# Kernel optimization log

Hardware: AMD Instinct MI355X
Metric: run time of the kernel (lower is better)

Reference implementation:

```python
import jax, jax.numpy as jnp
import numpy as np

B, T, D, F_FF, E, TOP_K = 8, 2048, 1024, 4096, 8, 2
CAP_FACTOR = 1.25


def setup_inputs() -> dict:
    key = jax.random.key(0)
    ks = jax.random.split(key, 7)
    s = 0.02
    return {
        "x": jax.random.normal(ks[0], (B, T, D), dtype=jnp.float32),
        "w_router": jax.random.normal(ks[1], (D, E), dtype=jnp.float32) * s,
        "b_router": jnp.zeros((E,), dtype=jnp.float32),
        "w1": jax.random.normal(ks[2], (E, D, F_FF), dtype=jnp.float32) * s,
        "b1": jnp.zeros((E, F_FF), dtype=jnp.float32),
        "w2": jax.random.normal(ks[3], (E, F_FF, D), dtype=jnp.float32) * s,
        "b2": jnp.zeros((E, D), dtype=jnp.float32),
    }


def reference(x, w_router, b_router, w1, b1, w2, b2):
    b, t, d = x.shape
    n = b * t
    e = w_router.shape[1]
    xf = x.reshape(n, d)

    # router in float32 (as original: .float())
    logits = xf.astype(jnp.float32) @ w_router + b_router
    gates = jax.nn.softmax(logits, axis=-1)              # [N, E]
    topv, topi = jax.lax.top_k(gates, TOP_K)             # [N, K]

    cap = max(1, int(CAP_FACTOR * n / e))

    # flatten assignments in (token, slot) order -> matches python loop order
    e_flat = topi.reshape(-1)                            # [N*K] expert id
    g_flat = topv.reshape(-1)                            # [N*K] gate value
    tok = jnp.repeat(jnp.arange(n), TOP_K)               # [N*K] token id

    # position of each assignment inside its expert (arrival order)
    onehot = jax.nn.one_hot(e_flat, e, dtype=jnp.int32)  # [N*K, E]
    pos = jnp.cumsum(onehot, axis=0)[jnp.arange(n * TOP_K), e_flat] - 1
    keep = pos < cap                                     # capacity dropping
    posc = jnp.minimum(pos, cap - 1)

    # dispatch: [E, cap, D] buffers (unique kept slots -> scatter-add safe)
    buf = jnp.zeros((e, cap, d), x.dtype).at[e_flat, posc].add(
        jnp.where(keep[:, None], xf[tok], 0.0))

    # per-expert FFN as grouped GEMM (exact GELU, as torch nn.GELU default)
    h = jax.nn.gelu(jnp.einsum('ecd,edf->ecf', buf, w1) + b1[:, None, :],
                    approximate=False)
    out = jnp.einsum('ecf,efd->ecd', h, w2) + b2[:, None, :]

    # combine: weighted scatter-add back to tokens
    og = out[e_flat, posc]                               # [N*K, D]
    w = jnp.where(keep, g_flat, 0.0).astype(x.dtype)
    y = jnp.zeros((n, d), x.dtype).at[tok].add(w[:, None] * og)
    ws = jnp.zeros((n,), x.dtype).at[tok].add(w)
    y = jnp.where((ws > 0.0)[:, None], y / jnp.maximum(ws, 1e-6)[:, None], y)
    return y.reshape(b, t, d)
```

## Files before the change

### kernel.cpp

```cpp
#include <hip/hip_runtime.h>

#define NTOK   16384
#define DMODEL 1024
#define FFF    4096
#define NEXP   8
#define CAP    2560
#define NASSIGN (NTOK*2)

typedef __bf16 bf16x8 __attribute__((ext_vector_type(8)));
typedef float  f32x4  __attribute__((ext_vector_type(4)));

__device__ __forceinline__ unsigned short f2bf(float f) {
    unsigned int u = __float_as_uint(f);
    u = u + 0x7FFFu + ((u >> 16) & 1u);
    return (unsigned short)(u >> 16);
}
__device__ __forceinline__ float bf2f(unsigned short s) {
    return __uint_as_float(((unsigned int)s) << 16);
}

__global__ void router_kernel(const float* __restrict__ x,
                              const float* __restrict__ wr,
                              const float* __restrict__ br,
                              int* __restrict__ topi,
                              float* __restrict__ topv) {
    int t    = blockIdx.x * 4 + (threadIdx.x >> 6);
    int lane = threadIdx.x & 63;
    const float* xr = x + (size_t)t * DMODEL;
    float a[8] = {0.f,0.f,0.f,0.f,0.f,0.f,0.f,0.f};
    for (int d = lane; d < DMODEL; d += 64) {
        float xv = xr[d];
        const float* w = wr + d * 8;
        #pragma unroll
        for (int e = 0; e < 8; e++) a[e] = fmaf(xv, w[e], a[e]);
    }
    #pragma unroll
    for (int off = 32; off > 0; off >>= 1) {
        #pragma unroll
        for (int e = 0; e < 8; e++) a[e] += __shfl_xor(a[e], off, 64);
    }
    if (lane == 0) {
        float l[8], g[8];
        float mx = -1e30f;
        #pragma unroll
        for (int e = 0; e < 8; e++) { l[e] = a[e] + br[e]; mx = fmaxf(mx, l[e]); }
        float s = 0.f;
        #pragma unroll
        for (int e = 0; e < 8; e++) { g[e] = expf(l[e] - mx); s += g[e]; }
        float inv = 1.f / s;
        #pragma unroll
        for (int e = 0; e < 8; e++) g[e] *= inv;
        float v1 = -1.f, v2 = -1.f; int i1 = 0, i2 = 0;
        #pragma unroll
        for (int e = 0; e < 8; e++) {
            float v = g[e];
            if (v > v1)      { v2 = v1; i2 = i1; v1 = v; i1 = e; }
            else if (v > v2) { v2 = v; i2 = e; }
        }
        topi[t*2]   = i1; topi[t*2+1] = i2;
        topv[t*2]   = v1; topv[t*2+1] = v2;
    }
}

__global__ void scan_kernel(const int* __restrict__ topi,
                            int* __restrict__ pos,
                            int* __restrict__ slot_tok,
                            int* __restrict__ kept) {
    const int APT = NASSIGN / 256;
    int tid = threadIdx.x, lane = tid & 63, w = tid >> 6;
    int base = tid * APT;
    int c[8] = {0,0,0,0,0,0,0,0};
    for (int i = 0; i < APT; i++) {
        int e = topi[base + i];
        #pragma unroll
        for (int q = 0; q < 8; q++) c[q] += (e == q);
    }
    int excl[8], wtot[8];
    #pragma unroll
    for (int e = 0; e < 8; e++) {
        int s = c[e];
        for (int off = 1; off < 64; off <<= 1) {
            int n = __shfl_up(s, off, 64);
            if (lane >= off) s += n;
        }
        excl[e] = s - c[e];
        wtot[e] = __shfl(s, 63, 64);
    }
    __shared__ int woff[4][8];
    if (lane == 0) {
        #pragma unroll
        for (int e = 0; e < 8; e++) woff[w][e] = wtot[e];
    }
    __syncthreads();
    if (tid == 0) {
        for (int e = 0; e < 8; e++) {
            int run = 0;
            for (int ww = 0; ww < 4; ww++) { int t0 = woff[ww][e]; woff[ww][e] = run; run += t0; }
            kept[e] = run < CAP ? run : CAP;
        }
    }
    __syncthreads();
    int run[8];
    #pragma unroll
    for (int e = 0; e < 8; e++) run[e] = woff[w][e] + excl[e];
    for (int i = 0; i < APT; i++) {
        int a = base + i;
        int e = topi[a];
        int p = 0;
        #pragma unroll
        for (int q = 0; q < 8; q++) if (e == q) { p = run[q]; run[q] = p + 1; }
        pos[a] = p;
        if (p < CAP) slot_tok[(size_t)e * CAP + p] = a >> 1;
    }
}

__global__ void dispatch_kernel(const float* __restrict__ x,
                                const int* __restrict__ slot_tok,
                                const int* __restrict__ kept,
                                unsigned short* __restrict__ xb) {
    int row  = blockIdx.x * 4 + (threadIdx.x >> 6);
    int lane = threadIdx.x & 63;
    int e = row / CAP;
    int p = row - e * CAP;
    if (p >= kept[e]) return;
    int t = slot_tok[row];
    const float4* src = reinterpret_cast<const float4*>(x + (size_t)t * DMODEL);
    ushort4* dst = reinterpret_cast<ushort4*>(xb + (size_t)row * DMODEL);
    #pragma unroll
    for (int i = lane; i < DMODEL/4; i += 64) {
        float4 v = src[i];
        ushort4 o;
        o.x = f2bf(v.x); o.y = f2bf(v.y); o.z = f2bf(v.z); o.w = f2bf(v.w);
        dst[i] = o;
    }
}

__global__ void transpose_f32_to_bf16(const float* __restrict__ in,
                                      unsigned short* __restrict__ out,
                                      int R, int C) {
    __shared__ float tile[32][33];
    int e = blockIdx.z;
    const float* src = in + (size_t)e * R * C;
    unsigned short* dst = out + (size_t)e * R * C;
    int c0 = blockIdx.x * 32, r0 = blockIdx.y * 32;
    #pragma unroll
    for (int i = threadIdx.y; i < 32; i += 8)
        tile[i][threadIdx.x] = src[(size_t)(r0 + i) * C + c0 + threadIdx.x];
    __syncthreads();
    #pragma unroll
    for (int i = threadIdx.y; i < 32; i += 8)
        dst[(size_t)(c0 + i) * R + r0 + threadIdx.x] = f2bf(tile[threadIdx.x][i]);
}

template<int GELU>
__global__ __launch_bounds__(256, 2)
void gemm_bt(const unsigned short* __restrict__ A,
             const unsigned short* __restrict__ Bt,
             const float* __restrict__ bias,
             unsigned short* __restrict__ C,
             int M, int N, int K) {
    constexpr int BM = 128, BN = 128, BK = 64, LDK = 72;
    __shared__ unsigned short As[BM * LDK];
    __shared__ unsigned short Bs[BN * LDK];
    const int e = blockIdx.z;
    const unsigned short* Ab = A  + (size_t)e * M * K + (size_t)blockIdx.y * BM * K;
    const unsigned short* Bb = Bt + (size_t)e * N * K + (size_t)blockIdx.x * BN * K;
    const float* bp = bias + (size_t)e * N;
    const int tid  = threadIdx.x;
    const int lane = tid & 63;
    const int wv   = tid >> 6;
    const int wm   = (wv >> 1) * 64;
    const int wn   = (wv & 1) * 64;
    const int lr   = lane & 15;
    const int quad = lane >> 4;
    const int sr   = tid >> 3;
    const int sc   = (tid & 7) * 8;

    f32x4 acc[4][4] = {};

    for (int kb = 0; kb < K; kb += BK) {
        #pragma unroll
        for (int s = 0; s < 4; s++) {
            int rr = sr + s * 32;
            *reinterpret_cast<uint4*>(&As[rr * LDK + sc]) =
                *reinterpret_cast<const uint4*>(Ab + (size_t)rr * K + kb + sc);
            *reinterpret_cast<uint4*>(&Bs[rr * LDK + sc]) =
                *reinterpret_cast<const uint4*>(Bb + (size_t)rr * K + kb + sc);
        }
        __syncthreads();
        #pragma unroll
        for (int kk = 0; kk < BK; kk += 32) {
            bf16x8 af[4], bfr[4];
            #pragma unroll
            for (int i = 0; i < 4; i++)
                af[i] = *reinterpret_cast<const bf16x8*>(&As[(wm + i*16 + lr) * LDK + kk + quad*8]);
            #pragma unroll
            for (int j = 0; j < 4; j++)
                bfr[j] = *reinterpret_cast<const bf16x8*>(&Bs[(wn + j*16 + lr) * LDK + kk + quad*8]);
            #pragma unroll
            for (int i = 0; i < 4; i++)
                #pragma unroll
                for (int j = 0; j < 4; j++)
                    acc[i][j] = __builtin_amdgcn_mfma_f32_16x16x32_bf16(af[i], bfr[j], acc[i][j], 0, 0, 0);
        }
        __syncthreads();
    }

    size_t cbase = (size_t)e * M * N + (size_t)blockIdx.y * BM * N + (size_t)blockIdx.x * BN;
    #pragma unroll
    for (int i = 0; i < 4; i++) {
        #pragma unroll
        for (int r = 0; r < 4; r++) {
            int row = wm + i * 16 + quad * 4 + r;
            #pragma unroll
            for (int j = 0; j < 4; j++) {
                int col = wn + j * 16 + lr;
                float v = acc[i][j][r] + bp[blockIdx.x * BN + col];
                if (GELU) v = 0.5f * v * (1.f + erff(v * 0.70710678118654752440f));
                C[cbase + (size_t)row * N + col] = f2bf(v);
            }
        }
    }
}

__global__ void combine_kernel(const int* __restrict__ topi,
                               const float* __restrict__ topv,
                               const int* __restrict__ pos,
                               const unsigned short* __restrict__ out2,
                               float* __restrict__ y) {
    int t    = blockIdx.x * 4 + (threadIdx.x >> 6);
    int lane = threadIdx.x & 63;
    int e0 = topi[t*2],   e1 = topi[t*2+1];
    float g0 = topv[t*2], g1 = topv[t*2+1];
    int p0 = pos[t*2],    p1 = pos[t*2+1];
    float w0 = (p0 < CAP) ? g0 : 0.f;
    float w1 = (p1 < CAP) ? g1 : 0.f;
    float wsum = w0 + w1;
    float scale = (wsum > 0.f) ? 1.f / fmaxf(wsum, 1e-6f) : 0.f;
    int q0 = p0 < CAP ? p0 : CAP - 1;
    int q1 = p1 < CAP ? p1 : CAP - 1;
    const ushort4* o0 = reinterpret_cast<const ushort4*>(out2 + ((size_t)e0 * CAP + q0) * DMODEL);
    const ushort4* o1 = reinterpret_cast<const ushort4*>(out2 + ((size_t)e1 * CAP + q1) * DMODEL);
    float4* dst = reinterpret_cast<float4*>(y + (size_t)t * DMODEL);
    #pragma unroll
    for (int i = lane; i < DMODEL/4; i += 64) {
        ushort4 a = o0[i], b = o1[i];
        float4 r;
        r.x = (w0 * bf2f(a.x) + w1 * bf2f(b.x)) * scale;
        r.y = (w0 * bf2f(a.y) + w1 * bf2f(b.y)) * scale;
        r.z = (w0 * bf2f(a.z) + w1 * bf2f(b.z)) * scale;
        r.w = (w0 * bf2f(a.w) + w1 * bf2f(b.w)) * scale;
        dst[i] = r;
    }
}

extern "C" void kernel_launch(void* const* d_in, const int* in_sizes, int n_in,
                              void* d_out, int out_size, void* d_ws, size_t ws_size,
                              hipStream_t stream) {
    (void)in_sizes; (void)n_in; (void)out_size; (void)ws_size;
    const float* x        = (const float*)d_in[0];
    const float* w_router = (const float*)d_in[1];
    const float* b_router = (const float*)d_in[2];
    const float* w1       = (const float*)d_in[3];
    const float* b1       = (const float*)d_in[4];
    const float* w2       = (const float*)d_in[5];
    const float* b2       = (const float*)d_in[6];
    float* y = (float*)d_out;

    char* ws = (char*)d_ws;
    size_t off = 0;
    auto alloc = [&](size_t n) { char* p = ws + off; off = (off + n + 255) & ~(size_t)255; return p; };
    int*   topi     = (int*)  alloc((size_t)NASSIGN * 4);
    float* topv     = (float*)alloc((size_t)NASSIGN * 4);
    int*   pos      = (int*)  alloc((size_t)NASSIGN * 4);
    int*   slot_tok = (int*)  alloc((size_t)NEXP * CAP * 4);
    int*   kept     = (int*)  alloc(8 * 4);
    unsigned short* w1t = (unsigned short*)alloc((size_t)NEXP * DMODEL * FFF * 2);
    unsigned short* w2t = (unsigned short*)alloc((size_t)NEXP * DMODEL * FFF * 2);
    unsigned short* xb  = (unsigned short*)alloc((size_t)NEXP * CAP * DMODEL * 2);
    unsigned short* h   = (unsigned short*)alloc((size_t)NEXP * CAP * FFF * 2);
    unsigned short* out2 = w1t;

    router_kernel<<<NTOK/4, 256, 0, stream>>>(x, w_router, b_router, topi, topv);
    scan_kernel<<<1, 256, 0, stream>>>(topi, pos, slot_tok, kept);
    dispatch_kernel<<<NEXP*CAP/4, 256, 0, stream>>>(x, slot_tok, kept, xb);
    transpose_f32_to_bf16<<<dim3(FFF/32, DMODEL/32, NEXP), dim3(32, 8), 0, stream>>>(w1, w1t, DMODEL, FFF);
    transpose_f32_to_bf16<<<dim3(DMODEL/32, FFF/32, NEXP), dim3(32, 8), 0, stream>>>(w2, w2t, FFF, DMODEL);
    gemm_bt<1><<<dim3(FFF/128, CAP/128, NEXP), 256, 0, stream>>>(xb, w1t, b1, h, CAP, FFF, DMODEL);
    gemm_bt<0><<<dim3(DMODEL/128, CAP/128, NEXP), 256, 0, stream>>>(h, w2t, b2, out2, CAP, DMODEL, FFF);
    combine_kernel<<<NTOK/4, 256, 0, stream>>>(topi, topv, pos, out2, y);
}
```

Before: 0.9997 ms.

## Use direct global-to-LDS loads with XOR swizzle in GEMM and vectorize helper kernels

The GEMM tile loads now go straight from global memory into LDS through global_load_lds, and the LDS layout uses an XOR swizzle in place of a padded stride. Bias values are hoisted out of the epilogue loop. The weight transpose now works on 64x64 tiles with float4 reads and 16-byte bf16 writes, and the router and scan kernels read their inputs as float4/int4. These changes aim to cut register staging, LDS bank conflicts and narrow memory accesses across several kernels, at the cost of relying on correct swizzle and row mapping for the direct LDS loads.

```diff
diff --git a/kernel.cpp b/kernel.cpp
--- a/kernel.cpp
+++ b/kernel.cpp
@@ -9,6 +9,7 @@
 
 typedef __bf16 bf16x8 __attribute__((ext_vector_type(8)));
 typedef float  f32x4  __attribute__((ext_vector_type(4)));
+typedef unsigned short u16x8 __attribute__((ext_vector_type(8)));
 
 __device__ __forceinline__ unsigned short f2bf(float f) {
     unsigned int u = __float_as_uint(f);
@@ -26,13 +27,20 @@
                               float* __restrict__ topv) {
     int t    = blockIdx.x * 4 + (threadIdx.x >> 6);
     int lane = threadIdx.x & 63;
-    const float* xr = x + (size_t)t * DMODEL;
+    const float4* xr4 = reinterpret_cast<const float4*>(x + (size_t)t * DMODEL);
     float a[8] = {0.f,0.f,0.f,0.f,0.f,0.f,0.f,0.f};
-    for (int d = lane; d < DMODEL; d += 64) {
-        float xv = xr[d];
-        const float* w = wr + d * 8;
-        #pragma unroll
-        for (int e = 0; e < 8; e++) a[e] = fmaf(xv, w[e], a[e]);
+    #pragma unroll
+    for (int i = lane; i < DMODEL/4; i += 64) {
+        float4 xv = xr4[i];
+        const float* w = wr + i * 32;
+        #pragma unroll
+        for (int e = 0; e < 8; e++) a[e] = fmaf(xv.x, w[e],      a[e]);
+        #pragma unroll
+        for (int e = 0; e < 8; e++) a[e] = fmaf(xv.y, w[8 + e],  a[e]);
+        #pragma unroll
+        for (int e = 0; e < 8; e++) a[e] = fmaf(xv.z, w[16 + e], a[e]);
+        #pragma unroll
+        for (int e = 0; e < 8; e++) a[e] = fmaf(xv.w, w[24 + e], a[e]);
     }
     #pragma unroll
     for (int off = 32; off > 0; off >>= 1) {
@@ -69,11 +77,13 @@
     const int APT = NASSIGN / 256;
     int tid = threadIdx.x, lane = tid & 63, w = tid >> 6;
     int base = tid * APT;
+    const int4* tp = reinterpret_cast<const int4*>(topi + base);
     int c[8] = {0,0,0,0,0,0,0,0};
-    for (int i = 0; i < APT; i++) {
-        int e = topi[base + i];
-        #pragma unroll
-        for (int q = 0; q < 8; q++) c[q] += (e == q);
+    for (int i = 0; i < APT/4; i++) {
+        int4 v = tp[i];
+        #pragma unroll
+        for (int q = 0; q < 8; q++)
+            c[q] += (v.x == q) + (v.y == q) + (v.z == q) + (v.w == q);
     }
     int excl[8], wtot[8];
     #pragma unroll
@@ -103,14 +113,19 @@
     int run[8];
     #pragma unroll
     for (int e = 0; e < 8; e++) run[e] = woff[w][e] + excl[e];
-    for (int i = 0; i < APT; i++) {
-        int a = base + i;
-        int e = topi[a];
-        int p = 0;
-        #pragma unroll
-        for (int q = 0; q < 8; q++) if (e == q) { p = run[q]; run[q] = p + 1; }
-        pos[a] = p;
-        if (p < CAP) slot_tok[(size_t)e * CAP + p] = a >> 1;
+    for (int i = 0; i < APT/4; i++) {
+        int4 v = tp[i];
+        int ev[4] = {v.x, v.y, v.z, v.w};
+        #pragma unroll
+        for (int u = 0; u < 4; u++) {
+            int a = base + i*4 + u;
+            int e = ev[u];
+            int p = 0;
+            #pragma unroll
+            for (int q = 0; q < 8; q++) if (e == q) { p = run[q]; run[q] = p + 1; }
+            pos[a] = p;
+            if (p < CAP) slot_tok[(size_t)e * CAP + p] = a >> 1;
+        }
     }
 }
 
@@ -138,18 +153,31 @@
 __global__ void transpose_f32_to_bf16(const float* __restrict__ in,
                                       unsigned short* __restrict__ out,
                                       int R, int C) {
-    __shared__ float tile[32][33];
+    __shared__ float tile[64 * 65];
     int e = blockIdx.z;
     const float* src = in + (size_t)e * R * C;
     unsigned short* dst = out + (size_t)e * R * C;
-    int c0 = blockIdx.x * 32, r0 = blockIdx.y * 32;
-    #pragma unroll
-    for (int i = threadIdx.y; i < 32; i += 8)
-        tile[i][threadIdx.x] = src[(size_t)(r0 + i) * C + c0 + threadIdx.x];
+    int c0 = blockIdx.x * 64, r0 = blockIdx.y * 64;
+    int t = threadIdx.x;
+    int lr4 = (t & 15) * 4;
+    #pragma unroll
+    for (int s = 0; s < 4; s++) {
+        int r = (t >> 4) + s * 16;
+        float4 v = *reinterpret_cast<const float4*>(&src[(size_t)(r0 + r) * C + c0 + lr4]);
+        float* tr = &tile[r * 65 + lr4];
+        tr[0] = v.x; tr[1] = v.y; tr[2] = v.z; tr[3] = v.w;
+    }
     __syncthreads();
-    #pragma unroll
-    for (int i = threadIdx.y; i < 32; i += 8)
-        dst[(size_t)(c0 + i) * R + r0 + threadIdx.x] = f2bf(tile[threadIdx.x][i]);
+    int j = t & 7;
+    int ccb = t >> 3;
+    #pragma unroll
+    for (int s = 0; s < 2; s++) {
+        int cc = ccb + s * 32;
+        u16x8 o;
+        #pragma unroll
+        for (int k = 0; k < 8; k++) o[k] = f2bf(tile[(j * 8 + k) * 65 + cc]);
+        *reinterpret_cast<u16x8*>(&dst[(size_t)(c0 + cc) * R + r0 + j * 8]) = o;
+    }
 }
 
 template<int GELU>
@@ -159,9 +187,9 @@
              const float* __restrict__ bias,
              unsigned short* __restrict__ C,
              int M, int N, int K) {
-    constexpr int BM = 128, BN = 128, BK = 64, LDK = 72;
-    __shared__ unsigned short As[BM * LDK];
-    __shared__ unsigned short Bs[BN * LDK];
+    constexpr int BM = 128, BN = 128, BK = 64;
+    __shared__ unsigned short As[BM * 64];
+    __shared__ unsigned short Bs[BN * 64];
     const int e = blockIdx.z;
     const unsigned short* Ab = A  + (size_t)e * M * K + (size_t)blockIdx.y * BM * K;
     const unsigned short* Bb = Bt + (size_t)e * N * K + (size_t)blockIdx.x * BN * K;
@@ -173,30 +201,37 @@
     const int wn   = (wv & 1) * 64;
     const int lr   = lane & 15;
     const int quad = lane >> 4;
-    const int sr   = tid >> 3;
-    const int sc   = (tid & 7) * 8;
+    const int srow   = lane >> 3;
+    const int schunk = (lane & 7) ^ srow;
+    const int swiz   = lr & 7;
 
     f32x4 acc[4][4] = {};
 
     for (int kb = 0; kb < K; kb += BK) {
         #pragma unroll
         for (int s = 0; s < 4; s++) {
-            int rr = sr + s * 32;
-            *reinterpret_cast<uint4*>(&As[rr * LDK + sc]) =
-                *reinterpret_cast<const uint4*>(Ab + (size_t)rr * K + kb + sc);
-            *reinterpret_cast<uint4*>(&Bs[rr * LDK + sc]) =
-                *reinterpret_cast<const uint4*>(Bb + (size_t)rr * K + kb + sc);
+            int q = wv * 4 + s;
+            int row = q * 8 + srow;
+            __builtin_amdgcn_global_load_lds(
+                (const __attribute__((address_space(1))) unsigned int*)(Ab + (size_t)row * K + kb + schunk * 8),
+                (__attribute__((address_space(3))) unsigned int*)(As + q * 512),
+                16, 0, 0);
+            __builtin_amdgcn_global_load_lds(
+                (const __attribute__((address_space(1))) unsigned int*)(Bb + (size_t)row * K + kb + schunk * 8),
+                (__attribute__((address_space(3))) unsigned int*)(Bs + q * 512),
+                16, 0, 0);
         }
         __syncthreads();
         #pragma unroll
         for (int kk = 0; kk < BK; kk += 32) {
             bf16x8 af[4], bfr[4];
+            const int sc = ((kk >> 3) + quad) ^ swiz;
             #pragma unroll
             for (int i = 0; i < 4; i++)
-                af[i] = *reinterpret_cast<const bf16x8*>(&As[(wm + i*16 + lr) * LDK + kk + quad*8]);
+                af[i] = *reinterpret_cast<const bf16x8*>(&As[(wm + i*16 + lr) * 64 + sc * 8]);
             #pragma unroll
             for (int j = 0; j < 4; j++)
-                bfr[j] = *reinterpret_cast<const bf16x8*>(&Bs[(wn + j*16 + lr) * LDK + kk + quad*8]);
+                bfr[j] = *reinterpret_cast<const bf16x8*>(&Bs[(wn + j*16 + lr) * 64 + sc * 8]);
             #pragma unroll
             for (int i = 0; i < 4; i++)
                 #pragma unroll
@@ -207,6 +242,9 @@
     }
 
     size_t cbase = (size_t)e * M * N + (size_t)blockIdx.y * BM * N + (size_t)blockIdx.x * BN;
+    float bv[4];
+    #pragma unroll
+    for (int j = 0; j < 4; j++) bv[j] = bp[blockIdx.x * BN + wn + j * 16 + lr];
     #pragma unroll
     for (int i = 0; i < 4; i++) {
         #pragma unroll
@@ -215,7 +253,7 @@
             #pragma unroll
             for (int j = 0; j < 4; j++) {
                 int col = wn + j * 16 + lr;
-                float v = acc[i][j][r] + bp[blockIdx.x * BN + col];
+                float v = acc[i][j][r] + bv[j];
                 if (GELU) v = 0.5f * v * (1.f + erff(v * 0.70710678118654752440f));
                 C[cbase + (size_t)row * N + col] = f2bf(v);
             }
@@ -284,8 +322,8 @@
     router_kernel<<<NTOK/4, 256, 0, stream>>>(x, w_router, b_router, topi, topv);
     scan_kernel<<<1, 256, 0, stream>>>(topi, pos, slot_tok, kept);
     dispatch_kernel<<<NEXP*CAP/4, 256, 0, stream>>>(x, slot_tok, kept, xb);
-    transpose_f32_to_bf16<<<dim3(FFF/32, DMODEL/32, NEXP), dim3(32, 8), 0, stream>>>(w1, w1t, DMODEL, FFF);
-    transpose_f32_to_bf16<<<dim3(DMODEL/32, FFF/32, NEXP), dim3(32, 8), 0, stream>>>(w2, w2t, FFF, DMODEL);
+    transpose_f32_to_bf16<<<dim3(FFF/64, DMODEL/64, NEXP), 256, 0, stream>>>(w1, w1t, DMODEL, FFF);
+    transpose_f32_to_bf16<<<dim3(DMODEL/64, FFF/64, NEXP), 256, 0, stream>>>(w2, w2t, FFF, DMODEL);
     gemm_bt<1><<<dim3(FFF/128, CAP/128, NEXP), 256, 0, stream>>>(xb, w1t, b1, h, CAP, FFF, DMODEL);
     gemm_bt<0><<<dim3(DMODEL/128, CAP/128, NEXP), 256, 0, stream>>>(h, w2t, b2, out2, CAP, DMODEL, FFF);
     combine_kernel<<<NTOK/4, 256, 0, stream>>>(topi, topv, pos, out2, y);
```

After: 914.6 us. 1.09x faster.
